# Kernel tuning notes

Hardware: AMD Instinct MI355X
Metric: run time of the kernel (lower is better)

## Reference

```python
import jax, jax.numpy as jnp
import numpy as np

N_NODES = 500_000
N_EDGES = 16_000_000
GCN_DIMS = [1, 4, 7, 10, 16]   # gcn layer in/out widths
MLP_DIMS = [16, 32, 16, 16]    # fc1, fc2, fc3 (raw_feature_size=16)


def setup_inputs() -> dict:
    key = jax.random.key(0)
    ks = list(jax.random.split(key, 40))
    ki = iter(ks)
    inp = {}
    inp["x"] = jax.random.normal(next(ki), (N_NODES, 1), dtype=jnp.float32)
    inp["edge_index"] = jax.random.randint(next(ki), (2, N_EDGES), 0, N_NODES, dtype=jnp.int32)
    # GraphConv params: lin_rel (weight+bias) applied to aggregated neighbors,
    # lin_root (weight, no bias) applied to self features.
    for li in range(4):
        din, dout = GCN_DIMS[li], GCN_DIMS[li + 1]
        s = 1.0 / np.sqrt(din)
        inp[f"g{li+1}_Wrel"] = jax.random.uniform(next(ki), (din, dout), jnp.float32, -s, s)
        inp[f"g{li+1}_brel"] = jax.random.uniform(next(ki), (dout,), jnp.float32, -s, s)
        inp[f"g{li+1}_Wroot"] = jax.random.uniform(next(ki), (din, dout), jnp.float32, -s, s)
    for li in range(3):
        din, dout = MLP_DIMS[li], MLP_DIMS[li + 1]
        s = 1.0 / np.sqrt(din)
        inp[f"fc{li+1}_W"] = jax.random.uniform(next(ki), (din, dout), jnp.float32, -s, s)
        inp[f"fc{li+1}_b"] = jax.random.uniform(next(ki), (dout,), jnp.float32, -s, s)
    return inp


def _graph_conv(x, Wrel, brel, Wroot, src, dst):
    # PyG GraphConv, aggr='add': out_i = Wrel @ (sum_{j->i} x_j) + brel + Wroot @ x_i
    agg = jax.ops.segment_sum(x[src], dst, num_segments=N_NODES)  # [N, din]
    return agg @ Wrel + brel + x @ Wroot


def reference(x, edge_index,
              g1_Wrel, g1_brel, g1_Wroot,
              g2_Wrel, g2_brel, g2_Wroot,
              g3_Wrel, g3_brel, g3_Wroot,
              g4_Wrel, g4_brel, g4_Wroot,
              fc1_W, fc1_b, fc2_W, fc2_b, fc3_W, fc3_b):
    src, dst = edge_index[0], edge_index[1]
    h = jax.nn.relu(_graph_conv(x, g1_Wrel, g1_brel, g1_Wroot, src, dst))
    h = jax.nn.relu(_graph_conv(h, g2_Wrel, g2_brel, g2_Wroot, src, dst))
    h = jax.nn.relu(_graph_conv(h, g3_Wrel, g3_brel, g3_Wroot, src, dst))
    h = jax.nn.relu(_graph_conv(h, g4_Wrel, g4_brel, g4_Wroot, src, dst))
    h = jax.nn.relu(h @ fc1_W + fc1_b)
    h = jax.nn.relu(h @ fc2_W + fc2_b)
    return h @ fc3_W + fc3_b
```

## Files before the change

kernel.cpp:

```cpp
#include <hip/hip_runtime.h>
#include <hip/hip_fp16.h>

#define N_NODES 500000
#define N_EDGES 16000000

#define SB_BITS 13
#define SB_SIZE (1 << SB_BITS)
#define NSUPER ((N_NODES + SB_SIZE - 1) / SB_SIZE)
#define CAP1 270336
#define BKT_BITS 9
#define BKT_SIZE (1 << BKT_BITS)
#define NBUCKET ((N_NODES + BKT_SIZE - 1) / BKT_SIZE)
#define BKT_CAP 17408
#define QBITS 2
#define NKEY (BKT_SIZE << QBITS)
#define B1_EPT 256
#define B1_CHUNK (256 * B1_EPT)
#define B1_NBLK ((N_EDGES + B1_CHUNK - 1) / B1_CHUNK)
#define B1_VQ (B1_EPT / 4)
#define NV4 (N_EDGES / 4)
#define B2_PER_SUPER 8

typedef unsigned int u32x2 __attribute__((ext_vector_type(2)));
typedef unsigned int u32x4 __attribute__((ext_vector_type(4)));
typedef float f32x2 __attribute__((ext_vector_type(2)));
typedef float f32x4 __attribute__((ext_vector_type(4)));

__device__ __forceinline__ unsigned int h2u(__half2 h) { return *(unsigned int*)&h; }
__device__ __forceinline__ float2 u2f2(unsigned int u) { return __half22float2(*(__half2*)&u); }

__global__ __launch_bounds__(512) void init_bcur_kernel(
    int* __restrict__ bcur1, int* __restrict__ bcur2)
{
    int i = blockIdx.x * 512 + threadIdx.x;
    if (i < NSUPER) bcur1[i] = i * CAP1;
    if (i < NBUCKET) bcur2[i] = i * BKT_CAP;
}

__global__ __launch_bounds__(256) void bin1_kernel(
    const int* __restrict__ src, const int* __restrict__ dst,
    int* __restrict__ bcur1, unsigned int* __restrict__ pairs1)
{
    __shared__ int lh[NSUPER];
    __shared__ int lbase[NSUPER];
    const int4* dst4 = (const int4*)dst;
    const int4* src4 = (const int4*)src;
    int t = threadIdx.x;
    long v0 = (long)blockIdx.x * (B1_CHUNK / 4);

    if (t < NSUPER) lh[t] = 0;
    __syncthreads();

#pragma unroll 8
    for (int q = 0; q < B1_VQ; ++q) {
        long v = v0 + q * 256 + t;
        if (v < NV4) {
            int4 d = dst4[v];
            atomicAdd(&lh[d.x >> SB_BITS], 1);
            atomicAdd(&lh[d.y >> SB_BITS], 1);
            atomicAdd(&lh[d.z >> SB_BITS], 1);
            atomicAdd(&lh[d.w >> SB_BITS], 1);
        }
    }
    __syncthreads();

    if (t < NSUPER) {
        int c = lh[t];
        lbase[t] = c ? atomicAdd(&bcur1[t], c) : 0;
        lh[t] = 0;
    }
    __syncthreads();

#pragma unroll 8
    for (int q = 0; q < B1_VQ; ++q) {
        long v = v0 + q * 256 + t;
        if (v < NV4) {
            int4 d = dst4[v];
            int4 s = src4[v];
            {
                int b = d.x >> SB_BITS;
                int r = atomicAdd(&lh[b], 1);
                pairs1[lbase[b] + r] = ((unsigned int)s.x << SB_BITS) | (unsigned int)(d.x & (SB_SIZE - 1));
            }
            {
                int b = d.y >> SB_BITS;
                int r = atomicAdd(&lh[b], 1);
                pairs1[lbase[b] + r] = ((unsigned int)s.y << SB_BITS) | (unsigned int)(d.y & (SB_SIZE - 1));
            }
            {
                int b = d.z >> SB_BITS;
                int r = atomicAdd(&lh[b], 1);
                pairs1[lbase[b] + r] = ((unsigned int)s.z << SB_BITS) | (unsigned int)(d.z & (SB_SIZE - 1));
            }
            {
                int b = d.w >> SB_BITS;
                int r = atomicAdd(&lh[b], 1);
                pairs1[lbase[b] + r] = ((unsigned int)s.w << SB_BITS) | (unsigned int)(d.w & (SB_SIZE - 1));
            }
        }
    }
}

__global__ __launch_bounds__(256) void bin2_kernel(
    const int* __restrict__ bcur1, int* __restrict__ bcur2,
    const unsigned int* __restrict__ pairs1, unsigned int* __restrict__ pairs2)
{
    __shared__ int lh[16];
    __shared__ int lbase[16];
    int s = blockIdx.x >> 3;
    int blk = blockIdx.x & 7;
    int t = threadIdx.x;
    int count = bcur1[s] - s * CAP1;
    int chunk = (((count + B2_PER_SUPER - 1) / B2_PER_SUPER) + 3) & ~3;
    int lo = blk * chunk;
    int hi = lo + chunk; if (hi > count) hi = count;
    int len = hi > lo ? hi - lo : 0;
    const unsigned int* base = pairs1 + (size_t)s * CAP1 + lo;
    const uint4* p4 = (const uint4*)base;
    int nv = len >> 2;

    if (t < 16) lh[t] = 0;
    __syncthreads();

    for (int i = t; i < nv; i += 256) {
        uint4 p = p4[i];
        atomicAdd(&lh[(p.x & (SB_SIZE - 1)) >> BKT_BITS], 1);
        atomicAdd(&lh[(p.y & (SB_SIZE - 1)) >> BKT_BITS], 1);
        atomicAdd(&lh[(p.z & (SB_SIZE - 1)) >> BKT_BITS], 1);
        atomicAdd(&lh[(p.w & (SB_SIZE - 1)) >> BKT_BITS], 1);
    }
    if (t < (len & 3))
        atomicAdd(&lh[(base[(nv << 2) + t] & (SB_SIZE - 1)) >> BKT_BITS], 1);
    __syncthreads();

    if (t < 16) {
        int c = lh[t];
        lbase[t] = c ? atomicAdd(&bcur2[(s << 4) | t], c) : 0;
        lh[t] = 0;
    }
    __syncthreads();

    for (int i = t; i < nv; i += 256) {
        uint4 p = p4[i];
#pragma unroll
        for (int q = 0; q < 4; ++q) {
            unsigned int e = (q == 0) ? p.x : (q == 1) ? p.y : (q == 2) ? p.z : p.w;
            int sub = (int)((e & (SB_SIZE - 1)) >> BKT_BITS);
            int r = atomicAdd(&lh[sub], 1);
            pairs2[lbase[sub] + r] = ((e >> SB_BITS) << BKT_BITS) | (e & (BKT_SIZE - 1));
        }
    }
    if (t < (len & 3)) {
        unsigned int e = base[(nv << 2) + t];
        int sub = (int)((e & (SB_SIZE - 1)) >> BKT_BITS);
        int r = atomicAdd(&lh[sub], 1);
        pairs2[lbase[sub] + r] = ((e >> SB_BITS) << BKT_BITS) | (e & (BKT_SIZE - 1));
    }
}

__global__ __launch_bounds__(512) void bucket_scan_kernel(
    const int* __restrict__ bcur2, int* __restrict__ bbase)
{
    __shared__ int sdata[512];
    int t = threadIdx.x;
    int i0 = t * 2;
    int v0 = (i0 < NBUCKET) ? (bcur2[i0] - i0 * BKT_CAP) : 0;
    int v1 = (i0 + 1 < NBUCKET) ? (bcur2[i0 + 1] - (i0 + 1) * BKT_CAP) : 0;
    int s = v0 + v1;
    sdata[t] = s;
    __syncthreads();
    for (int o = 1; o < 512; o <<= 1) {
        int tmp = (t >= o) ? sdata[t - o] : 0;
        __syncthreads();
        sdata[t] += tmp;
        __syncthreads();
    }
    int run = sdata[t] - s;
    if (i0 < NBUCKET) bbase[i0] = run;
    if (i0 + 1 < NBUCKET) bbase[i0 + 1] = run + v0;
    if (i0 == NBUCKET - 1) bbase[NBUCKET] = run + v0;
    if (i0 + 1 == NBUCKET - 1) bbase[NBUCKET] = run + v0 + v1;
}

__global__ __launch_bounds__(512) void bucket_sort512_kernel(
    const int* __restrict__ bcur2, const int* __restrict__ bbase,
    const unsigned int* __restrict__ pairs2, const float* __restrict__ xfeat,
    int* __restrict__ off4, int* __restrict__ sorted_src,
    float* __restrict__ agg1)
{
    __shared__ int   stage[BKT_CAP];
    __shared__ int   lh[NKEY];
    __shared__ float laccum[BKT_SIZE];
    int b = blockIdx.x;
    int t = threadIdx.x;
    int base_node = b << BKT_BITS;
    size_t pstart = (size_t)b * BKT_CAP;
    int count = bcur2[b] - b * BKT_CAP;
    int cstart = bbase[b];

    lh[t] = 0; lh[512 + t] = 0; lh[1024 + t] = 0; lh[1536 + t] = 0;
    laccum[t & (BKT_SIZE - 1)] = 0.0f;
    __syncthreads();

    int nv = count >> 2;
    const uint4* p4 = (const uint4*)(pairs2 + pstart);
    for (int i = t; i < nv; i += 512) {
        uint4 p = p4[i];
        atomicAdd(&lh[((p.x & (BKT_SIZE - 1)) << QBITS) | (p.x >> 26)], 1);
        atomicAdd(&lh[((p.y & (BKT_SIZE - 1)) << QBITS) | (p.y >> 26)], 1);
        atomicAdd(&lh[((p.z & (BKT_SIZE - 1)) << QBITS) | (p.z >> 26)], 1);
        atomicAdd(&lh[((p.w & (BKT_SIZE - 1)) << QBITS) | (p.w >> 26)], 1);
    }
    if (t < (count & 3)) {
        unsigned int pe = pairs2[pstart + (nv << 2) + t];
        atomicAdd(&lh[((pe & (BKT_SIZE - 1)) << QBITS) | (pe >> 26)], 1);
    }
    __syncthreads();

    int i0 = t * 4;
    int c0 = lh[i0], c1 = lh[i0 + 1], c2 = lh[i0 + 2], c3 = lh[i0 + 3];
    int s = c0 + c1 + c2 + c3;
    stage[t] = s;
    __syncthreads();
    for (int o = 1; o < 512; o <<= 1) {
        int tmp = (t >= o) ? stage[t - o] : 0;
        __syncthreads();
        stage[t] += tmp;
        __syncthreads();
    }
    int run = cstart + stage[t] - s;
    int vals[4] = {c0, c1, c2, c3};
#pragma unroll
    for (int q = 0; q < 4; ++q) {
        int key = i0 + q;
        int node = base_node + (key >> QBITS);
        if (node < N_NODES) {
            off4[(size_t)base_node * 4 + key] = run;
            if (node == N_NODES - 1 && (key & 3) == 3)
                off4[(size_t)N_NODES * 4] = run + vals[q];
        }
        lh[key] = run;
        run += vals[q];
    }
    __syncthreads();

    for (int i = t; i < nv; i += 512) {
        uint4 p = p4[i];
#pragma unroll
        for (int q = 0; q < 4; ++q) {
            unsigned int pe = (q == 0) ? p.x : (q == 1) ? p.y : (q == 2) ? p.z : p.w;
            int key = (int)(((pe & (BKT_SIZE - 1)) << QBITS) | (pe >> 26));
            int sidx = (int)(pe >> BKT_BITS);
            int pos = atomicAdd(&lh[key], 1);
            stage[pos - cstart] = sidx;
            atomicAdd(&laccum[pe & (BKT_SIZE - 1)], xfeat[sidx]);
        }
    }
    if (t < (count & 3)) {
        unsigned int pe = pairs2[pstart + (nv << 2) + t];
        int key = (int)(((pe & (BKT_SIZE - 1)) << QBITS) | (pe >> 26));
        int sidx = (int)(pe >> BKT_BITS);
        int pos = atomicAdd(&lh[key], 1);
        stage[pos - cstart] = sidx;
        atomicAdd(&laccum[pe & (BKT_SIZE - 1)], xfeat[sidx]);
    }
    __syncthreads();

    for (int j = t; j < count; j += 512)
        __builtin_nontemporal_store(stage[j], &sorted_src[cstart + j]);
    int node = base_node + t;
    if (node < N_NODES) __builtin_nontemporal_store(laccum[t], &agg1[node]);
}

__global__ __launch_bounds__(256) void transform1_kernel(
    const float* __restrict__ agg1, const float* __restrict__ x,
    const float* __restrict__ Wrel, const float* __restrict__ brel,
    const float* __restrict__ Wroot,
    __half2* __restrict__ h1)
{
    __shared__ float w[12];
    if (threadIdx.x < 4) {
        w[threadIdx.x] = Wrel[threadIdx.x];
        w[4 + threadIdx.x] = brel[threadIdx.x];
        w[8 + threadIdx.x] = Wroot[threadIdx.x];
    }
    __syncthreads();
    int i = blockIdx.x * blockDim.x + threadIdx.x;
    if (i >= N_NODES) return;
    float a = agg1[i], xv = x[i];
    float r0 = fmaxf(a * w[0] + w[4] + xv * w[8],  0.0f);
    float r1 = fmaxf(a * w[1] + w[5] + xv * w[9],  0.0f);
    float r2 = fmaxf(a * w[2] + w[6] + xv * w[10], 0.0f);
    float r3 = fmaxf(a * w[3] + w[7] + xv * w[11], 0.0f);
    u32x2 v = { h2u(__floats2half2_rn(r0, r1)), h2u(__floats2half2_rn(r2, r3)) };
    __builtin_nontemporal_store(v, (u32x2*)(h1 + (size_t)i * 2));
}

__global__ __launch_bounds__(256) void gather2t_kernel(
    const int* __restrict__ off4, const int* __restrict__ ss,
    const __half2* __restrict__ h1,
    const float* __restrict__ Wrel, const float* __restrict__ brel,
    const float* __restrict__ Wroot,
    __half2* __restrict__ h2)
{
    __shared__ float tile[128 * 5];
    __shared__ float sWr[28], sWo[28], sb[7];
    int t = threadIdx.x;
    if (t < 28) { sWr[t] = Wrel[t]; sWo[t] = Wroot[t]; }
    if (t < 7) sb[t] = brel[t];

    int ln = t >> 1;
    int j = t & 1;
    int node = blockIdx.x * 128 + ln;
    if (node < N_NODES) {
        int start = off4[(size_t)node * 4], end = off4[(size_t)node * 4 + 4];
        float a0x=0,a0y=0,a1x=0,a1y=0,a2x=0,a2y=0,a3x=0,a3y=0;
        float b0x=0,b0y=0,b1x=0,b1y=0,b2x=0,b2y=0,b3x=0,b3y=0;
        int e = start;
        for (; e + 8 <= end; e += 8) {
            int s0=ss[e],s1=ss[e+1],s2=ss[e+2],s3=ss[e+3];
            int s4=ss[e+4],s5=ss[e+5],s6=ss[e+6],s7=ss[e+7];
            float2 f0=__half22float2(h1[(size_t)s0*2+j]);
            float2 f1=__half22float2(h1[(size_t)s1*2+j]);
            float2 f2=__half22float2(h1[(size_t)s2*2+j]);
            float2 f3=__half22float2(h1[(size_t)s3*2+j]);
            float2 f4=__half22float2(h1[(size_t)s4*2+j]);
            float2 f5=__half22float2(h1[(size_t)s5*2+j]);
            float2 f6=__half22float2(h1[(size_t)s6*2+j]);
            float2 f7=__half22float2(h1[(size_t)s7*2+j]);
            a0x+=f0.x;a0y+=f0.y; a1x+=f1.x;a1y+=f1.y;
            a2x+=f2.x;a2y+=f2.y; a3x+=f3.x;a3y+=f3.y;
            b0x+=f4.x;b0y+=f4.y; b1x+=f5.x;b1y+=f5.y;
            b2x+=f6.x;b2y+=f6.y; b3x+=f7.x;b3y+=f7.y;
        }
        for (; e < end; ++e) {
            float2 f = __half22float2(h1[(size_t)ss[e]*2+j]);
            a0x += f.x; a0y += f.y;
        }
        float rx = ((a0x+a1x)+(a2x+a3x)) + ((b0x+b1x)+(b2x+b3x));
        float ry = ((a0y+a1y)+(a2y+a3y)) + ((b0y+b1y)+(b2y+b3y));
        tile[ln * 5 + 2 * j] = rx;
        tile[ln * 5 + 2 * j + 1] = ry;
    }
    __syncthreads();

    if (t < 128) {
        int n2 = blockIdx.x * 128 + t;
        if (n2 < N_NODES) {
            float av[4];
#pragma unroll
            for (int k = 0; k < 4; ++k) av[k] = tile[t * 5 + k];
            float2 x01 = __half22float2(h1[(size_t)n2 * 2]);
            float2 x23 = __half22float2(h1[(size_t)n2 * 2 + 1]);
            float xv[4] = {x01.x, x01.y, x23.x, x23.y};
            float o_[8];
#pragma unroll
            for (int o = 0; o < 7; ++o) {
                float v = sb[o];
#pragma unroll
                for (int k = 0; k < 4; ++k)
                    v += av[k] * sWr[k * 7 + o] + xv[k] * sWo[k * 7 + o];
                o_[o] = fmaxf(v, 0.0f);
            }
            o_[7] = 0.0f;
            u32x4 v = { h2u(__floats2half2_rn(o_[0], o_[1])),
                        h2u(__floats2half2_rn(o_[2], o_[3])),
                        h2u(__floats2half2_rn(o_[4], o_[5])),
                        h2u(__floats2half2_rn(o_[6], o_[7])) };
            __builtin_nontemporal_store(v, (u32x4*)(h2 + (size_t)n2 * 4));
        }
    }
}

__global__ __launch_bounds__(256) void gather3t_kernel(
    const int* __restrict__ off4, const int* __restrict__ ss,
    const __half2* __restrict__ h2,
    const float* __restrict__ Wrel, const float* __restrict__ brel,
    const float* __restrict__ Wroot,
    __half2* __restrict__ h3)
{
    __shared__ float tile[64 * 9];
    __shared__ float sWr[70], sWo[70], sb[10];
    int t = threadIdx.x;
    if (t < 70) { sWr[t] = Wrel[t]; sWo[t] = Wroot[t]; }
    if (t < 10) sb[t] = brel[t];

    int ln = t >> 2;
    int j = t & 3;
    int node = blockIdx.x * 64 + ln;
    if (node < N_NODES) {
        int start = off4[(size_t)node * 4], end = off4[(size_t)node * 4 + 4];
        float a0x=0,a0y=0,a1x=0,a1y=0,a2x=0,a2y=0,a3x=0,a3y=0;
        float b0x=0,b0y=0,b1x=0,b1y=0,b2x=0,b2y=0,b3x=0,b3y=0;
        int e = start;
        for (; e + 8 <= end; e += 8) {
            int s0=ss[e],s1=ss[e+1],s2=ss[e+2],s3=ss[e+3];
            int s4=ss[e+4],s5=ss[e+5],s6=ss[e+6],s7=ss[e+7];
            float2 f0=__half22float2(h2[(size_t)s0*4+j]);
            float2 f1=__half22float2(h2[(size_t)s1*4+j]);
            float2 f2=__half22float2(h2[(size_t)s2*4+j]);
            float2 f3=__half22float2(h2[(size_t)s3*4+j]);
            float2 f4=__half22float2(h2[(size_t)s4*4+j]);
            float2 f5=__half22float2(h2[(size_t)s5*4+j]);
            float2 f6=__half22float2(h2[(size_t)s6*4+j]);
            float2 f7=__half22float2(h2[(size_t)s7*4+j]);
            a0x+=f0.x;a0y+=f0.y; a1x+=f1.x;a1y+=f1.y;
            a2x+=f2.x;a2y+=f2.y; a3x+=f3.x;a3y+=f3.y;
            b0x+=f4.x;b0y+=f4.y; b1x+=f5.x;b1y+=f5.y;
            b2x+=f6.x;b2y+=f6.y; b3x+=f7.x;b3y+=f7.y;
        }
        for (; e < end; ++e) {
            float2 f = __half22float2(h2[(size_t)ss[e]*4+j]);
            a0x += f.x; a0y += f.y;
        }
        float rx = ((a0x+a1x)+(a2x+a3x)) + ((b0x+b1x)+(b2x+b3x));
        float ry = ((a0y+a1y)+(a2y+a3y)) + ((b0y+b1y)+(b2y+b3y));
        tile[ln * 9 + 2 * j] = rx;
        tile[ln * 9 + 2 * j + 1] = ry;
    }
    __syncthreads();

    if (t < 64) {
        int n2 = blockIdx.x * 64 + t;
        if (n2 < N_NODES) {
            float av[7];
#pragma unroll
            for (int k = 0; k < 7; ++k) av[k] = tile[t * 9 + k];
            float xv[8];
#pragma unroll
            for (int q = 0; q < 4; ++q) {
                float2 f = __half22float2(h2[(size_t)n2 * 4 + q]);
                xv[2 * q] = f.x; xv[2 * q + 1] = f.y;
            }
            float o_[16];
#pragma unroll
            for (int o = 0; o < 10; ++o) {
                float v = sb[o];
#pragma unroll
                for (int k = 0; k < 7; ++k)
                    v += av[k] * sWr[k * 10 + o] + xv[k] * sWo[k * 10 + o];
                o_[o] = fmaxf(v, 0.0f);
            }
#pragma unroll
            for (int o = 10; o < 16; ++o) o_[o] = 0.0f;
            u32x4 v0 = { h2u(__floats2half2_rn(o_[0], o_[1])),
                         h2u(__floats2half2_rn(o_[2], o_[3])),
                         h2u(__floats2half2_rn(o_[4], o_[5])),
                         h2u(__floats2half2_rn(o_[6], o_[7])) };
            u32x4 v1 = { h2u(__floats2half2_rn(o_[8], o_[9])),
                         h2u(__floats2half2_rn(o_[10], o_[11])),
                         h2u(__floats2half2_rn(o_[12], o_[13])),
                         h2u(__floats2half2_rn(o_[14], o_[15])) };
            __builtin_nontemporal_store(v0, (u32x4*)(h3 + (size_t)n2 * 8));
            __builtin_nontemporal_store(v1, (u32x4*)(h3 + (size_t)n2 * 8 + 4));
        }
    }
}

template<int Q>
__global__ __launch_bounds__(256) void gather4_kernel(
    const int* __restrict__ off4, const int* __restrict__ ss,
    const __half2* __restrict__ h3, float* __restrict__ agg)
{
    int node = blockIdx.x * 32 + (threadIdx.x >> 3);
    int j = threadIdx.x & 7;
    if (node >= N_NODES) return;
    int start = off4[(size_t)node * 4 + Q], end = off4[(size_t)node * 4 + Q + 1];

    float a0x=0,a0y=0,a1x=0,a1y=0,a2x=0,a2y=0,a3x=0,a3y=0;
    float b0x=0,b0y=0,b1x=0,b1y=0,b2x=0,b2y=0,b3x=0,b3y=0;
    int e = start;
    for (; e + 16 <= end; e += 16) {
        int s0=ss[e+0], s1=ss[e+1], s2=ss[e+2],  s3=ss[e+3];
        int s4=ss[e+4], s5=ss[e+5], s6=ss[e+6],  s7=ss[e+7];
        int s8=ss[e+8], s9=ss[e+9], sa=ss[e+10], sb=ss[e+11];
        int sc=ss[e+12],sd=ss[e+13],se=ss[e+14], sf=ss[e+15];
        float2 f0=__half22float2(h3[(size_t)s0*8+j]);
        float2 f1=__half22float2(h3[(size_t)s1*8+j]);
        float2 f2=__half22float2(h3[(size_t)s2*8+j]);
        float2 f3=__half22float2(h3[(size_t)s3*8+j]);
        float2 f4=__half22float2(h3[(size_t)s4*8+j]);
        float2 f5=__half22float2(h3[(size_t)s5*8+j]);
        float2 f6=__half22float2(h3[(size_t)s6*8+j]);
        float2 f7=__half22float2(h3[(size_t)s7*8+j]);
        float2 f8=__half22float2(h3[(size_t)s8*8+j]);
        float2 f9=__half22float2(h3[(size_t)s9*8+j]);
        float2 fa=__half22float2(h3[(size_t)sa*8+j]);
        float2 fb=__half22float2(h3[(size_t)sb*8+j]);
        float2 fc=__half22float2(h3[(size_t)sc*8+j]);
        float2 fd=__half22float2(h3[(size_t)sd*8+j]);
        float2 fe=__half22float2(h3[(size_t)se*8+j]);
        float2 ff=__half22float2(h3[(size_t)sf*8+j]);
        a0x+=f0.x;a0y+=f0.y; a1x+=f1.x;a1y+=f1.y;
        a2x+=f2.x;a2y+=f2.y; a3x+=f3.x;a3y+=f3.y;
        b0x+=f4.x;b0y+=f4.y; b1x+=f5.x;b1y+=f5.y;
        b2x+=f6.x;b2y+=f6.y; b3x+=f7.x;b3y+=f7.y;
        a0x+=f8.x;a0y+=f8.y; a1x+=f9.x;a1y+=f9.y;
        a2x+=fa.x;a2y+=fa.y; a3x+=fb.x;a3y+=fb.y;
        b0x+=fc.x;b0y+=fc.y; b1x+=fd.x;b1y+=fd.y;
        b2x+=fe.x;b2y+=fe.y; b3x+=ff.x;b3y+=ff.y;
    }
    for (; e + 4 <= end; e += 4) {
        int s0=ss[e+0], s1=ss[e+1], s2=ss[e+2], s3=ss[e+3];
        float2 f0=__half22float2(h3[(size_t)s0*8+j]);
        float2 f1=__half22float2(h3[(size_t)s1*8+j]);
        float2 f2=__half22float2(h3[(size_t)s2*8+j]);
        float2 f3=__half22float2(h3[(size_t)s3*8+j]);
        a0x+=f0.x;a0y+=f0.y; a1x+=f1.x;a1y+=f1.y;
        a2x+=f2.x;a2y+=f2.y; a3x+=f3.x;a3y+=f3.y;
    }
    for (; e < end; ++e) {
        float2 f = __half22float2(h3[(size_t)ss[e]*8+j]);
        a0x += f.x; a0y += f.y;
    }
    float rx = ((a0x+a1x)+(a2x+a3x)) + ((b0x+b1x)+(b2x+b3x));
    float ry = ((a0y+a1y)+(a2y+a3y)) + ((b0y+b1y)+(b2y+b3y));
    float* dst = agg + (size_t)node * 16 + j * 2;
    if (Q == 0) {
        f32x2 v = { rx, ry };
        __builtin_nontemporal_store(v, (f32x2*)dst);
    } else {
        f32x2 v = *(const f32x2*)dst;
        v[0] += rx; v[1] += ry;
        __builtin_nontemporal_store(v, (f32x2*)dst);
    }
}

__global__ __launch_bounds__(256) void layer4_mlp_kernel(
    const float* __restrict__ agg, const __half2* __restrict__ h3,
    const float* __restrict__ g4Wrel, const float* __restrict__ g4brel,
    const float* __restrict__ g4Wroot,
    const float* __restrict__ fc1W, const float* __restrict__ fc1b,
    const float* __restrict__ fc2W, const float* __restrict__ fc2b,
    const float* __restrict__ fc3W, const float* __restrict__ fc3b,
    float* __restrict__ out)
{
    __shared__ float s[1680];
    float* sWrel  = s;
    float* sbrel  = s + 160;
    float* sWroot = s + 176;
    float* sfc1W  = s + 336;
    float* sfc1b  = s + 848;
    float* sfc2W  = s + 880;
    float* sfc2b  = s + 1392;
    float* sfc3W  = s + 1408;
    float* sfc3b  = s + 1664;
    int t = threadIdx.x;
    for (int i = t; i < 160; i += 256) { sWrel[i] = g4Wrel[i]; sWroot[i] = g4Wroot[i]; }
    for (int i = t; i < 512; i += 256) { sfc1W[i] = fc1W[i]; sfc2W[i] = fc2W[i]; }
    if (t < 256) sfc3W[t] = fc3W[t];
    if (t < 32)  sfc1b[t] = fc1b[t];
    if (t < 16)  { sbrel[t] = g4brel[t]; sfc2b[t] = fc2b[t]; sfc3b[t] = fc3b[t]; }
    __syncthreads();

    int i = blockIdx.x * blockDim.x + threadIdx.x;
    if (i >= N_NODES) return;

    const float4* ap = (const float4*)(agg + (size_t)i * 16);
    float4 a0 = ap[0], a1 = ap[1], a2 = ap[2];
    float a[10] = {a0.x, a0.y, a0.z, a0.w, a1.x, a1.y, a1.z, a1.w, a2.x, a2.y};
    float xin[10];
#pragma unroll
    for (int q = 0; q < 5; ++q) {
        float2 f = __half22float2(h3[(size_t)i * 8 + q]);
        xin[2 * q] = f.x; xin[2 * q + 1] = f.y;
    }

    float h4[16];
#pragma unroll
    for (int o = 0; o < 16; ++o) {
        float v = sbrel[o];
#pragma unroll
        for (int k = 0; k < 10; ++k)
            v += a[k] * sWrel[k * 16 + o] + xin[k] * sWroot[k * 16 + o];
        h4[o] = fmaxf(v, 0.0f);
    }
    float m1[32];
#pragma unroll
    for (int o = 0; o < 32; ++o) {
        float v = sfc1b[o];
#pragma unroll
        for (int k = 0; k < 16; ++k) v += h4[k] * sfc1W[k * 32 + o];
        m1[o] = fmaxf(v, 0.0f);
    }
    float m2[16];
#pragma unroll
    for (int o = 0; o < 16; ++o) {
        float v = sfc2b[o];
#pragma unroll
        for (int k = 0; k < 32; ++k) v += m1[k] * sfc2W[k * 16 + o];
        m2[o] = fmaxf(v, 0.0f);
    }
    float r[16];
#pragma unroll
    for (int o = 0; o < 16; ++o) {
        float v = sfc3b[o];
#pragma unroll
        for (int k = 0; k < 16; ++k) v += m2[k] * sfc3W[k * 16 + o];
        r[o] = v;
    }
#pragma unroll
    for (int q = 0; q < 4; ++q) {
        f32x4 v = { r[q*4+0], r[q*4+1], r[q*4+2], r[q*4+3] };
        __builtin_nontemporal_store(v, (f32x4*)(out + (size_t)i * 16 + q * 4));
    }
}

extern "C" void kernel_launch(void* const* d_in, const int* in_sizes, int n_in,
                              void* d_out, int out_size, void* d_ws, size_t ws_size,
                              hipStream_t stream) {
    const float* x        = (const float*)d_in[0];
    const int*   ei       = (const int*)d_in[1];
    const float* g1_Wrel  = (const float*)d_in[2];
    const float* g1_brel  = (const float*)d_in[3];
    const float* g1_Wroot = (const float*)d_in[4];
    const float* g2_Wrel  = (const float*)d_in[5];
    const float* g2_brel  = (const float*)d_in[6];
    const float* g2_Wroot = (const float*)d_in[7];
    const float* g3_Wrel  = (const float*)d_in[8];
    const float* g3_brel  = (const float*)d_in[9];
    const float* g3_Wroot = (const float*)d_in[10];
    const float* g4_Wrel  = (const float*)d_in[11];
    const float* g4_brel  = (const float*)d_in[12];
    const float* g4_Wroot = (const float*)d_in[13];
    const float* fc1_W    = (const float*)d_in[14];
    const float* fc1_b    = (const float*)d_in[15];
    const float* fc2_W    = (const float*)d_in[16];
    const float* fc2_b    = (const float*)d_in[17];
    const float* fc3_W    = (const float*)d_in[18];
    const float* fc3_b    = (const float*)d_in[19];
    float* out = (float*)d_out;

    const int* srcp = ei;
    const int* dstp = ei + N_EDGES;

    char* p = (char*)d_ws;
    auto alloc = [&](size_t bytes) {
        char* r = p;
        p += (bytes + 255) & ~(size_t)255;
        return r;
    };
    __half2* h1  = (__half2*)alloc((size_t)N_NODES * 2 * sizeof(__half2));
    __half2* h2  = (__half2*)alloc((size_t)N_NODES * 4 * sizeof(__half2));
    __half2* h3  = (__half2*)alloc((size_t)N_NODES * 8 * sizeof(__half2));
    float*   agg = (float*)  alloc((size_t)N_NODES * 16 * 4);
    alloc((size_t)14 * 1024 * 1024);
    unsigned int* pairs2 = (unsigned int*)h1;
    int* sorted_src = (int*)alloc((size_t)NSUPER * CAP1 * 4);
    unsigned int* pairs1 = (unsigned int*)sorted_src;
    int*   off4  = (int*)alloc(((size_t)N_NODES * 4 + 1) * 4);
    float* agg1  = (float*)alloc((size_t)N_NODES * 4);
    int*   bcur1 = (int*)alloc((size_t)NSUPER * 4);
    int*   bcur2 = (int*)alloc((size_t)NBUCKET * 4);
    int*   bbase = (int*)alloc((size_t)(NBUCKET + 1) * 4);

    const int TB = 256;
    const int node_blocks = (N_NODES + TB - 1) / TB;

    init_bcur_kernel<<<2, 512, 0, stream>>>(bcur1, bcur2);
    bin1_kernel<<<B1_NBLK, 256, 0, stream>>>(srcp, dstp, bcur1, pairs1);
    bin2_kernel<<<NSUPER * B2_PER_SUPER, 256, 0, stream>>>(bcur1, bcur2, pairs1, pairs2);
    bucket_scan_kernel<<<1, 512, 0, stream>>>(bcur2, bbase);
    bucket_sort512_kernel<<<NBUCKET, 512, 0, stream>>>(
        bcur2, bbase, pairs2, x, off4, sorted_src, agg1);

    transform1_kernel<<<node_blocks, TB, 0, stream>>>(
        agg1, x, g1_Wrel, g1_brel, g1_Wroot, h1);

    gather2t_kernel<<<(N_NODES + 127) / 128, TB, 0, stream>>>(
        off4, sorted_src, h1, g2_Wrel, g2_brel, g2_Wroot, h2);
    gather3t_kernel<<<(N_NODES + 63) / 64, TB, 0, stream>>>(
        off4, sorted_src, h2, g3_Wrel, g3_brel, g3_Wroot, h3);

    const int g4_blocks = (N_NODES + 31) / 32;
    gather4_kernel<0><<<g4_blocks, TB, 0, stream>>>(off4, sorted_src, h3, agg);
    gather4_kernel<1><<<g4_blocks, TB, 0, stream>>>(off4, sorted_src, h3, agg);
    gather4_kernel<2><<<g4_blocks, TB, 0, stream>>>(off4, sorted_src, h3, agg);
    gather4_kernel<3><<<g4_blocks, TB, 0, stream>>>(off4, sorted_src, h3, agg);
    layer4_mlp_kernel<<<node_blocks, TB, 0, stream>>>(
        agg, h3, g4_Wrel, g4_brel, g4_Wroot,
        fc1_W, fc1_b, fc2_W, fc2_b, fc3_W, fc3_b, out);
}
```

Before: 877.5 us.

## Split layer-3 gather into four source-quarter passes plus separate transform

Replaces the fused layer-3 gather+transform kernel with four gather passes, each covering one quarter of every node's edges (the ranges given by off4), accumulating into an fp32 agg buffer. A separate transform kernel then applies the weights. Like the existing layer-4 scheme, this keeps each pass's random reads of h2 within a smaller source range so they hit cache more often. The cost is extra launches, a read-modify-write of agg on each pass, and an added round trip through agg before the transform.

```diff
diff --git a/kernel.cpp b/kernel.cpp
--- a/kernel.cpp
+++ b/kernel.cpp
@@ -372,89 +372,118 @@
     }
 }
 
-__global__ __launch_bounds__(256) void gather3t_kernel(
+template<int Q>
+__global__ __launch_bounds__(256) void gather3_kernel(
     const int* __restrict__ off4, const int* __restrict__ ss,
-    const __half2* __restrict__ h2,
+    const __half2* __restrict__ h2, float* __restrict__ agg)
+{
+    int node = blockIdx.x * 64 + (threadIdx.x >> 2);
+    int j = threadIdx.x & 3;
+    if (node >= N_NODES) return;
+    int start = off4[(size_t)node * 4 + Q], end = off4[(size_t)node * 4 + Q + 1];
+
+    float a0x=0,a0y=0,a1x=0,a1y=0,a2x=0,a2y=0,a3x=0,a3y=0;
+    float b0x=0,b0y=0,b1x=0,b1y=0,b2x=0,b2y=0,b3x=0,b3y=0;
+    int e = start;
+    for (; e + 16 <= end; e += 16) {
+        int s0=ss[e+0], s1=ss[e+1], s2=ss[e+2],  s3=ss[e+3];
+        int s4=ss[e+4], s5=ss[e+5], s6=ss[e+6],  s7=ss[e+7];
+        int s8=ss[e+8], s9=ss[e+9], sa=ss[e+10], sb=ss[e+11];
+        int sc=ss[e+12],sd=ss[e+13],se=ss[e+14], sf=ss[e+15];
+        float2 f0=__half22float2(h2[(size_t)s0*4+j]);
+        float2 f1=__half22float2(h2[(size_t)s1*4+j]);
+        float2 f2=__half22float2(h2[(size_t)s2*4+j]);
+        float2 f3=__half22float2(h2[(size_t)s3*4+j]);
+        float2 f4=__half22float2(h2[(size_t)s4*4+j]);
+        float2 f5=__half22float2(h2[(size_t)s5*4+j]);
+        float2 f6=__half22float2(h2[(size_t)s6*4+j]);
+        float2 f7=__half22float2(h2[(size_t)s7*4+j]);
+        float2 f8=__half22float2(h2[(size_t)s8*4+j]);
+        float2 f9=__half22float2(h2[(size_t)s9*4+j]);
+        float2 fa=__half22float2(h2[(size_t)sa*4+j]);
+        float2 fb=__half22float2(h2[(size_t)sb*4+j]);
+        float2 fc=__half22float2(h2[(size_t)sc*4+j]);
+        float2 fd=__half22float2(h2[(size_t)sd*4+j]);
+        float2 fe=__half22float2(h2[(size_t)se*4+j]);
+        float2 ff=__half22float2(h2[(size_t)sf*4+j]);
+        a0x+=f0.x;a0y+=f0.y; a1x+=f1.x;a1y+=f1.y;
+        a2x+=f2.x;a2y+=f2.y; a3x+=f3.x;a3y+=f3.y;
+        b0x+=f4.x;b0y+=f4.y; b1x+=f5.x;b1y+=f5.y;
+        b2x+=f6.x;b2y+=f6.y; b3x+=f7.x;b3y+=f7.y;
+        a0x+=f8.x;a0y+=f8.y; a1x+=f9.x;a1y+=f9.y;
+        a2x+=fa.x;a2y+=fa.y; a3x+=fb.x;a3y+=fb.y;
+        b0x+=fc.x;b0y+=fc.y; b1x+=fd.x;b1y+=fd.y;
+        b2x+=fe.x;b2y+=fe.y; b3x+=ff.x;b3y+=ff.y;
+    }
+    for (; e + 4 <= end; e += 4) {
+        int s0=ss[e+0], s1=ss[e+1], s2=ss[e+2], s3=ss[e+3];
+        float2 f0=__half22float2(h2[(size_t)s0*4+j]);
+        float2 f1=__half22float2(h2[(size_t)s1*4+j]);
+        float2 f2=__half22float2(h2[(size_t)s2*4+j]);
+        float2 f3=__half22float2(h2[(size_t)s3*4+j]);
+        a0x+=f0.x;a0y+=f0.y; a1x+=f1.x;a1y+=f1.y;
+        a2x+=f2.x;a2y+=f2.y; a3x+=f3.x;a3y+=f3.y;
+    }
+    for (; e < end; ++e) {
+        float2 f = __half22float2(h2[(size_t)ss[e]*4+j]);
+        a0x += f.x; a0y += f.y;
+    }
+    float rx = ((a0x+a1x)+(a2x+a3x)) + ((b0x+b1x)+(b2x+b3x));
+    float ry = ((a0y+a1y)+(a2y+a3y)) + ((b0y+b1y)+(b2y+b3y));
+    float* dst = agg + (size_t)node * 8 + j * 2;
+    if (Q == 0) {
+        f32x2 v = { rx, ry };
+        __builtin_nontemporal_store(v, (f32x2*)dst);
+    } else {
+        f32x2 v = *(const f32x2*)dst;
+        v[0] += rx; v[1] += ry;
+        __builtin_nontemporal_store(v, (f32x2*)dst);
+    }
+}
+
+__global__ __launch_bounds__(256) void transform3_kernel(
+    const float* __restrict__ agg, const __half2* __restrict__ h2,
     const float* __restrict__ Wrel, const float* __restrict__ brel,
     const float* __restrict__ Wroot,
     __half2* __restrict__ h3)
 {
-    __shared__ float tile[64 * 9];
     __shared__ float sWr[70], sWo[70], sb[10];
     int t = threadIdx.x;
     if (t < 70) { sWr[t] = Wrel[t]; sWo[t] = Wroot[t]; }
     if (t < 10) sb[t] = brel[t];
-
-    int ln = t >> 2;
-    int j = t & 3;
-    int node = blockIdx.x * 64 + ln;
-    if (node < N_NODES) {
-        int start = off4[(size_t)node * 4], end = off4[(size_t)node * 4 + 4];
-        float a0x=0,a0y=0,a1x=0,a1y=0,a2x=0,a2y=0,a3x=0,a3y=0;
-        float b0x=0,b0y=0,b1x=0,b1y=0,b2x=0,b2y=0,b3x=0,b3y=0;
-        int e = start;
-        for (; e + 8 <= end; e += 8) {
-            int s0=ss[e],s1=ss[e+1],s2=ss[e+2],s3=ss[e+3];
-            int s4=ss[e+4],s5=ss[e+5],s6=ss[e+6],s7=ss[e+7];
-            float2 f0=__half22float2(h2[(size_t)s0*4+j]);
-            float2 f1=__half22float2(h2[(size_t)s1*4+j]);
-            float2 f2=__half22float2(h2[(size_t)s2*4+j]);
-            float2 f3=__half22float2(h2[(size_t)s3*4+j]);
-            float2 f4=__half22float2(h2[(size_t)s4*4+j]);
-            float2 f5=__half22float2(h2[(size_t)s5*4+j]);
-            float2 f6=__half22float2(h2[(size_t)s6*4+j]);
-            float2 f7=__half22float2(h2[(size_t)s7*4+j]);
-            a0x+=f0.x;a0y+=f0.y; a1x+=f1.x;a1y+=f1.y;
-            a2x+=f2.x;a2y+=f2.y; a3x+=f3.x;a3y+=f3.y;
-            b0x+=f4.x;b0y+=f4.y; b1x+=f5.x;b1y+=f5.y;
-            b2x+=f6.x;b2y+=f6.y; b3x+=f7.x;b3y+=f7.y;
-        }
-        for (; e < end; ++e) {
-            float2 f = __half22float2(h2[(size_t)ss[e]*4+j]);
-            a0x += f.x; a0y += f.y;
-        }
-        float rx = ((a0x+a1x)+(a2x+a3x)) + ((b0x+b1x)+(b2x+b3x));
-        float ry = ((a0y+a1y)+(a2y+a3y)) + ((b0y+b1y)+(b2y+b3y));
-        tile[ln * 9 + 2 * j] = rx;
-        tile[ln * 9 + 2 * j + 1] = ry;
-    }
-    __syncthreads();
-
-    if (t < 64) {
-        int n2 = blockIdx.x * 64 + t;
-        if (n2 < N_NODES) {
-            float av[7];
-#pragma unroll
-            for (int k = 0; k < 7; ++k) av[k] = tile[t * 9 + k];
-            float xv[8];
-#pragma unroll
-            for (int q = 0; q < 4; ++q) {
-                float2 f = __half22float2(h2[(size_t)n2 * 4 + q]);
-                xv[2 * q] = f.x; xv[2 * q + 1] = f.y;
-            }
-            float o_[16];
-#pragma unroll
-            for (int o = 0; o < 10; ++o) {
-                float v = sb[o];
-#pragma unroll
-                for (int k = 0; k < 7; ++k)
-                    v += av[k] * sWr[k * 10 + o] + xv[k] * sWo[k * 10 + o];
-                o_[o] = fmaxf(v, 0.0f);
-            }
-#pragma unroll
-            for (int o = 10; o < 16; ++o) o_[o] = 0.0f;
-            u32x4 v0 = { h2u(__floats2half2_rn(o_[0], o_[1])),
-                         h2u(__floats2half2_rn(o_[2], o_[3])),
-                         h2u(__floats2half2_rn(o_[4], o_[5])),
-                         h2u(__floats2half2_rn(o_[6], o_[7])) };
-            u32x4 v1 = { h2u(__floats2half2_rn(o_[8], o_[9])),
-                         h2u(__floats2half2_rn(o_[10], o_[11])),
-                         h2u(__floats2half2_rn(o_[12], o_[13])),
-                         h2u(__floats2half2_rn(o_[14], o_[15])) };
-            __builtin_nontemporal_store(v0, (u32x4*)(h3 + (size_t)n2 * 8));
-            __builtin_nontemporal_store(v1, (u32x4*)(h3 + (size_t)n2 * 8 + 4));
-        }
-    }
+    __syncthreads();
+    int i = blockIdx.x * blockDim.x + threadIdx.x;
+    if (i >= N_NODES) return;
+    const float4* ap = (const float4*)(agg + (size_t)i * 8);
+    float4 a0 = ap[0], a1 = ap[1];
+    float av[7] = {a0.x, a0.y, a0.z, a0.w, a1.x, a1.y, a1.z};
+    float xv[8];
+#pragma unroll
+    for (int q = 0; q < 4; ++q) {
+        float2 f = __half22float2(h2[(size_t)i * 4 + q]);
+        xv[2 * q] = f.x; xv[2 * q + 1] = f.y;
+    }
+    float o_[16];
+#pragma unroll
+    for (int o = 0; o < 10; ++o) {
+        float v = sb[o];
+#pragma unroll
+        for (int k = 0; k < 7; ++k)
+            v += av[k] * sWr[k * 10 + o] + xv[k] * sWo[k * 10 + o];
+        o_[o] = fmaxf(v, 0.0f);
+    }
+#pragma unroll
+    for (int o = 10; o < 16; ++o) o_[o] = 0.0f;
+    u32x4 v0 = { h2u(__floats2half2_rn(o_[0], o_[1])),
+                 h2u(__floats2half2_rn(o_[2], o_[3])),
+                 h2u(__floats2half2_rn(o_[4], o_[5])),
+                 h2u(__floats2half2_rn(o_[6], o_[7])) };
+    u32x4 v1 = { h2u(__floats2half2_rn(o_[8], o_[9])),
+                 h2u(__floats2half2_rn(o_[10], o_[11])),
+                 h2u(__floats2half2_rn(o_[12], o_[13])),
+                 h2u(__floats2half2_rn(o_[14], o_[15])) };
+    __builtin_nontemporal_store(v0, (u32x4*)(h3 + (size_t)i * 8));
+    __builtin_nontemporal_store(v1, (u32x4*)(h3 + (size_t)i * 8 + 4));
 }
 
 template<int Q>
@@ -669,8 +698,14 @@
 
     gather2t_kernel<<<(N_NODES + 127) / 128, TB, 0, stream>>>(
         off4, sorted_src, h1, g2_Wrel, g2_brel, g2_Wroot, h2);
-    gather3t_kernel<<<(N_NODES + 63) / 64, TB, 0, stream>>>(
-        off4, sorted_src, h2, g3_Wrel, g3_brel, g3_Wroot, h3);
+
+    const int g3_blocks = (N_NODES + 63) / 64;
+    gather3_kernel<0><<<g3_blocks, TB, 0, stream>>>(off4, sorted_src, h2, agg);
+    gather3_kernel<1><<<g3_blocks, TB, 0, stream>>>(off4, sorted_src, h2, agg);
+    gather3_kernel<2><<<g3_blocks, TB, 0, stream>>>(off4, sorted_src, h2, agg);
+    gather3_kernel<3><<<g3_blocks, TB, 0, stream>>>(off4, sorted_src, h2, agg);
+    transform3_kernel<<<node_blocks, TB, 0, stream>>>(
+        agg, h2, g3_Wrel, g3_brel, g3_Wroot, h3);
 
     const int g4_blocks = (N_NODES + 31) / 32;
     gather4_kernel<0><<<g4_blocks, TB, 0, stream>>>(off4, sorted_src, h3, agg);
```

New measurement: 850.3 us. 1.03x faster.
